# Kernel optimization log

Hardware: AMD Instinct MI355X
Metric: run time of the kernel (lower is better)

The kernel has to match this reference:

```python
import jax, jax.numpy as jnp
import numpy as np

NEG_SLOPE = 0.2
EPS = 1e-16  # matches PyG-style segment softmax denominator guard

N_NODES = 50000
N_EDGES = 800000
IN_CH = 256
HEADS = 4
OUT_CH = 32


def setup_inputs() -> dict:
    key = jax.random.key(0)
    k1, k2, k3, k4 = jax.random.split(key, 4)
    nodes_ft = jax.random.normal(k1, (N_NODES, IN_CH), dtype=jnp.float32)
    adj_list = jax.random.randint(k2, (2, N_EDGES), 0, N_NODES, dtype=jnp.int64)
    # xavier-normal-ish scales
    weight = jax.random.normal(k3, (IN_CH, HEADS * OUT_CH), dtype=jnp.float32) * (
        (2.0 / (IN_CH + HEADS * OUT_CH)) ** 0.5
    )
    att = jax.random.normal(k4, (1, HEADS, 2 * OUT_CH), dtype=jnp.float32) * (
        (2.0 / (1 + 2 * OUT_CH)) ** 0.5
    )
    bias = jnp.zeros((HEADS * OUT_CH,), dtype=jnp.float32)
    return {"nodes_ft": nodes_ft, "adj_list": adj_list, "weight": weight, "att": att, "bias": bias}


def reference(nodes_ft, adj_list, weight, att, bias):
    N = nodes_ft.shape[0]
    H, C = att.shape[1], att.shape[2] // 2
    dst = adj_list[0]  # softmax / aggregation key
    src = adj_list[1]
    # node hidden states: [N, H, C]
    h = (nodes_ft @ weight).reshape(N, H, C)
    xi = h[dst]  # [E, H, C]
    xj = h[src]  # [E, H, C]
    # attention logits: cat([xi, xj]) . att  ==  xi.att_i + xj.att_j
    att_i, att_j = att[:, :, :C], att[:, :, C:]
    alpha = (xi * att_i).sum(-1) + (xj * att_j).sum(-1)  # [E, H]
    alpha = jax.nn.leaky_relu(alpha, negative_slope=NEG_SLOPE)
    # segment softmax over destination node
    m = jax.ops.segment_max(alpha, dst, num_segments=N)  # [N, H]
    m = jnp.where(jnp.isfinite(m), m, 0.0)
    e = jnp.exp(alpha - m[dst])
    s = jax.ops.segment_sum(e, dst, num_segments=N)  # [N, H]
    a = e / (s[dst] + EPS)  # [E, H]
    # weighted scatter-add aggregate
    vals = xj * a[:, :, None]  # [E, H, C]
    out = jax.ops.segment_sum(vals, dst, num_segments=N)  # [N, H, C]
    out = out.reshape(N, H * C) + bias  # concat=True
    return out
```

## Files before the change

kernel.cpp:

```cpp
#include <hip/hip_runtime.h>
#include <hip/hip_bf16.h>
#include <math.h>

#define NN 50000
#define NE 800000
#define IN_CH 256
#define HEADS 4
#define OUT_CH 32
#define HC 128
#define NEG_SLOPE 0.2f
#define GAT_EPS 1e-16f

#define SBS 1024
#define NB  ((NN + SBS - 1) / SBS)

#define OFF_HB     0
#define OFF_WT     (NN*HC/2)
#define OFF_AI     (OFF_WT + 16384)
#define OFF_AJ     (OFF_AI + NN*HEADS)
#define OFF_ROW    (OFF_AJ + NN*HEADS)
#define OFF_CUR    (OFF_ROW + NN + 4)
#define OFF_HIST   (OFF_CUR + NN + 4)
#define OFF_BSUM   (OFF_HIST + NN + 4)
#define OFF_BOFF   (OFF_BSUM + NB + 4)
#define OFF_ESRC   (OFF_BOFF + NB + 4)

typedef __attribute__((ext_vector_type(8))) short short8v;
typedef __attribute__((ext_vector_type(4))) float float4v;

__device__ __forceinline__ unsigned short f2bf(float x) {
    union { float f; unsigned u; } v; v.f = x;
    unsigned r = v.u + 0x7fffu + ((v.u >> 16) & 1u);
    return (unsigned short)(r >> 16);
}
__device__ __forceinline__ float bf2f(unsigned short b) {
    union { unsigned u; float f; } v; v.u = ((unsigned)b) << 16;
    return v.f;
}

__global__ void k_zero(int* __restrict__ hist) {
    int i = blockIdx.x * blockDim.x + threadIdx.x;
    if (i < NN) hist[i] = 0;
}

__global__ void k_wt(const float* __restrict__ W, unsigned short* __restrict__ Wt) {
    int idx = blockIdx.x * blockDim.x + threadIdx.x;
    if (idx >= HC * IN_CH) return;
    int n = idx >> 8, k = idx & 255;
    Wt[n * IN_CH + k] = f2bf(W[(size_t)k * HC + n]);
}

__global__ __launch_bounds__(256) void k_gemm(const float* __restrict__ A,
                                              const unsigned short* __restrict__ Wt,
                                              unsigned short* __restrict__ Hb) {
    const int tid  = threadIdx.x;
    const int lane = tid & 63;
    const int w    = tid >> 6;
    const int wr   = w >> 1, wc = w & 1;
    const int blockRow = blockIdx.x * 128;

    const int lrow = lane & 15;
    const int kgrp = lane >> 4;

    float4v acc[4][4];
#pragma unroll
    for (int i = 0; i < 4; i++)
#pragma unroll
        for (int j = 0; j < 4; j++) acc[i][j] = (float4v){0.f, 0.f, 0.f, 0.f};

#pragma unroll
    for (int ks = 0; ks < 8; ks++) {
        const int kb = ks * 32 + kgrp * 8;
        short8v af[4], bfr[4];
#pragma unroll
        for (int mi = 0; mi < 4; mi++) {
            int r = blockRow + wr * 64 + mi * 16 + lrow;
            if (r >= NN) r = NN - 1;
            const float* ap = A + (size_t)r * IN_CH + kb;
            float4 a0 = *(const float4*)ap;
            float4 a1 = *(const float4*)(ap + 4);
            short8v t;
            t[0] = (short)f2bf(a0.x); t[1] = (short)f2bf(a0.y);
            t[2] = (short)f2bf(a0.z); t[3] = (short)f2bf(a0.w);
            t[4] = (short)f2bf(a1.x); t[5] = (short)f2bf(a1.y);
            t[6] = (short)f2bf(a1.z); t[7] = (short)f2bf(a1.w);
            af[mi] = t;
        }
#pragma unroll
        for (int ni = 0; ni < 4; ni++) {
            int c = wc * 64 + ni * 16 + lrow;
            bfr[ni] = *(const short8v*)(Wt + (size_t)c * IN_CH + kb);
        }
#pragma unroll
        for (int mi = 0; mi < 4; mi++)
#pragma unroll
            for (int ni = 0; ni < 4; ni++)
                acc[mi][ni] = __builtin_amdgcn_mfma_f32_16x16x32_bf16(
                    af[mi], bfr[ni], acc[mi][ni], 0, 0, 0);
    }

#pragma unroll
    for (int mi = 0; mi < 4; mi++) {
#pragma unroll
        for (int reg = 0; reg < 4; reg++) {
            int r = blockRow + wr * 64 + mi * 16 + kgrp * 4 + reg;
            if (r >= NN) continue;
#pragma unroll
            for (int ni = 0; ni < 4; ni++) {
                int c = wc * 64 + ni * 16 + lrow;
                Hb[(size_t)r * HC + c] = f2bf(acc[mi][ni][reg]);
            }
        }
    }
}

__global__ void k_att(const unsigned short* __restrict__ Hb, const float* __restrict__ att,
                      float* __restrict__ ai, float* __restrict__ aj) {
    int idx = blockIdx.x * blockDim.x + threadIdx.x;
    if (idx >= NN * HEADS) return;
    int n = idx >> 2, hh = idx & 3;
    const unsigned* hp = (const unsigned*)(Hb + (size_t)n * HC + hh * OUT_CH);
    const float* ati = att + hh * 2 * OUT_CH;
    const float* atj = ati + OUT_CH;
    float si = 0.f, sj = 0.f;
#pragma unroll
    for (int i = 0; i < 16; i++) {
        unsigned u = hp[i];
        float lo = bf2f((unsigned short)(u & 0xffff));
        float hi = bf2f((unsigned short)(u >> 16));
        si = fmaf(lo, ati[2 * i], si);     si = fmaf(hi, ati[2 * i + 1], si);
        sj = fmaf(lo, atj[2 * i], sj);     sj = fmaf(hi, atj[2 * i + 1], sj);
    }
    ai[idx] = si;
    aj[idx] = sj;
}

__global__ void k_hist(const int* __restrict__ adj, int* __restrict__ hist) {
    int e = blockIdx.x * blockDim.x + threadIdx.x;
    if (e < NE) atomicAdd(&hist[adj[e]], 1);
}

__global__ __launch_bounds__(256) void k_bsum(const int* __restrict__ hist,
                                              int* __restrict__ bsum) {
    int b = blockIdx.x, t = threadIdx.x;
    int i0 = b * SBS + t * 4;
    int s = 0;
#pragma unroll
    for (int j = 0; j < 4; j++) {
        int i = i0 + j;
        if (i < NN) s += hist[i];
    }
#pragma unroll
    for (int off = 32; off; off >>= 1) s += __shfl_xor(s, off);
    __shared__ int ws[4];
    int lane = t & 63, wid = t >> 6;
    if (lane == 0) ws[wid] = s;
    __syncthreads();
    if (t == 0) bsum[b] = ws[0] + ws[1] + ws[2] + ws[3];
}

__global__ __launch_bounds__(64) void k_bscan(const int* __restrict__ bsum,
                                              int* __restrict__ boff) {
    int lane = threadIdx.x;
    int v = (lane < NB) ? bsum[lane] : 0;
    int inc = v;
#pragma unroll
    for (int off = 1; off < 64; off <<= 1) {
        int u = __shfl_up(inc, off);
        if (lane >= off) inc += u;
    }
    if (lane < NB) boff[lane] = inc - v;
}

__global__ __launch_bounds__(256) void k_bwrite(const int* __restrict__ hist,
                                                const int* __restrict__ boff,
                                                int* __restrict__ row,
                                                int* __restrict__ cur) {
    int b = blockIdx.x, t = threadIdx.x;
    int i0 = b * SBS + t * 4;
    int v[4];
    int s = 0;
#pragma unroll
    for (int j = 0; j < 4; j++) {
        int i = i0 + j;
        v[j] = (i < NN) ? hist[i] : 0;
        s += v[j];
    }
    int lane = t & 63, wid = t >> 6;
    int inc = s;
#pragma unroll
    for (int off = 1; off < 64; off <<= 1) {
        int u = __shfl_up(inc, off);
        if (lane >= off) inc += u;
    }
    __shared__ int wsum[4];
    if (lane == 63) wsum[wid] = inc;
    __syncthreads();
    int woff = 0;
    for (int w2 = 0; w2 < wid; w2++) woff += wsum[w2];
    int run = boff[b] + woff + (inc - s);
#pragma unroll
    for (int j = 0; j < 4; j++) {
        int i = i0 + j;
        if (i < NN) {
            row[i] = run;
            cur[i] = run;
            run += v[j];
        }
    }
    if (b == 0 && t == 0) row[NN] = NE;
}

__global__ void k_scatter(const int* __restrict__ adj, int* __restrict__ cur,
                          int* __restrict__ esrc) {
    int e = blockIdx.x * blockDim.x + threadIdx.x;
    if (e >= NE) return;
    int dst = adj[e];
    int src = adj[NE + e];
    int pos = atomicAdd(&cur[dst], 1);
    esrc[pos] = src;
}

__device__ __forceinline__ float lrelu(float x) {
    return x > 0.f ? x : NEG_SLOPE * x;
}

__global__ __launch_bounds__(256) void k_gather(const int* __restrict__ row,
                                                const int* __restrict__ esrc,
                                                const float* __restrict__ ai,
                                                const float* __restrict__ aj,
                                                const unsigned short* __restrict__ Hb,
                                                const float* __restrict__ bias,
                                                float* __restrict__ out) {
    int gid = blockIdx.x * blockDim.x + threadIdx.x;
    int nid = gid >> 6;
    int lane = gid & 63;
    if (nid >= NN) return;
    int r0 = row[nid];
    int deg = row[nid + 1] - r0;

    float4 aiv = *(const float4*)&ai[nid * 4];

    float mx0 = -INFINITY, mx1 = -INFINITY, mx2 = -INFINITY, mx3 = -INFINITY;
    for (int k = lane; k < deg; k += 64) {
        int s = esrc[r0 + k];
        float4 ajv = *(const float4*)&aj[s * 4];
        mx0 = fmaxf(mx0, lrelu(aiv.x + ajv.x));
        mx1 = fmaxf(mx1, lrelu(aiv.y + ajv.y));
        mx2 = fmaxf(mx2, lrelu(aiv.z + ajv.z));
        mx3 = fmaxf(mx3, lrelu(aiv.w + ajv.w));
    }
#pragma unroll
    for (int off = 32; off; off >>= 1) {
        mx0 = fmaxf(mx0, __shfl_xor(mx0, off));
        mx1 = fmaxf(mx1, __shfl_xor(mx1, off));
        mx2 = fmaxf(mx2, __shfl_xor(mx2, off));
        mx3 = fmaxf(mx3, __shfl_xor(mx3, off));
    }

    float s0 = 0.f, s1 = 0.f, s2 = 0.f, s3 = 0.f;
    for (int k = lane; k < deg; k += 64) {
        int s = esrc[r0 + k];
        float4 ajv = *(const float4*)&aj[s * 4];
        s0 += __expf(lrelu(aiv.x + ajv.x) - mx0);
        s1 += __expf(lrelu(aiv.y + ajv.y) - mx1);
        s2 += __expf(lrelu(aiv.z + ajv.z) - mx2);
        s3 += __expf(lrelu(aiv.w + ajv.w) - mx3);
    }
#pragma unroll
    for (int off = 32; off; off >>= 1) {
        s0 += __shfl_xor(s0, off);
        s1 += __shfl_xor(s1, off);
        s2 += __shfl_xor(s2, off);
        s3 += __shfl_xor(s3, off);
    }

    int c0 = lane * 2;
    int hh = lane >> 4;
    float mh  = (hh & 2) ? ((hh & 1) ? mx3 : mx2) : ((hh & 1) ? mx1 : mx0);
    float sh  = (hh & 2) ? ((hh & 1) ? s3 : s2) : ((hh & 1) ? s1 : s0);
    float aih = (hh & 2) ? ((hh & 1) ? aiv.w : aiv.z) : ((hh & 1) ? aiv.y : aiv.x);
    float inv = 1.0f / (sh + GAT_EPS);

    float accx = 0.f, accy = 0.f;
#pragma unroll 4
    for (int k = 0; k < deg; k++) {
        int s = esrc[r0 + k];
        float al = lrelu(aih + aj[s * 4 + hh]);
        float a = __expf(al - mh) * inv;
        unsigned hu = *(const unsigned*)(Hb + (size_t)s * HC + c0);
        accx = fmaf(bf2f((unsigned short)(hu & 0xffff)), a, accx);
        accy = fmaf(bf2f((unsigned short)(hu >> 16)), a, accy);
    }
    out[(size_t)nid * HC + c0]     = accx + bias[c0];
    out[(size_t)nid * HC + c0 + 1] = accy + bias[c0 + 1];
}

extern "C" void kernel_launch(void* const* d_in, const int* in_sizes, int n_in,
                              void* d_out, int out_size, void* d_ws, size_t ws_size,
                              hipStream_t stream) {
    const float* nodes  = (const float*)d_in[0];
    const int*   adj    = (const int*)d_in[1];
    const float* weight = (const float*)d_in[2];
    const float* att    = (const float*)d_in[3];
    const float* bias   = (const float*)d_in[4];
    float* out = (float*)d_out;
    float* ws  = (float*)d_ws;

    unsigned short* Hb = (unsigned short*)(ws + OFF_HB);
    unsigned short* Wt = (unsigned short*)(ws + OFF_WT);
    float* ai   = ws + OFF_AI;
    float* aj   = ws + OFF_AJ;
    int*   rowp = (int*)(ws + OFF_ROW);
    int*   cur  = (int*)(ws + OFF_CUR);
    int*   hist = (int*)(ws + OFF_HIST);
    int*   bsum = (int*)(ws + OFF_BSUM);
    int*   boff = (int*)(ws + OFF_BOFF);
    int*   esrc = (int*)(ws + OFF_ESRC);

    k_zero<<<(NN + 255) / 256, 256, 0, stream>>>(hist);
    k_hist<<<(NE + 255) / 256, 256, 0, stream>>>(adj, hist);
    k_bsum<<<NB, 256, 0, stream>>>(hist, bsum);
    k_bscan<<<1, 64, 0, stream>>>(bsum, boff);
    k_bwrite<<<NB, 256, 0, stream>>>(hist, boff, rowp, cur);
    k_scatter<<<(NE + 255) / 256, 256, 0, stream>>>(adj, cur, esrc);
    k_wt<<<(HC * IN_CH + 255) / 256, 256, 0, stream>>>(weight, Wt);
    k_gemm<<<(NN + 127) / 128, 256, 0, stream>>>(nodes, Wt, Hb);
    k_att<<<(NN * HEADS + 255) / 256, 256, 0, stream>>>(Hb, att, ai, aj);
    k_gather<<<(NN * 64 + 255) / 256, 256, 0, stream>>>(rowp, esrc, ai, aj, Hb, bias, out);
}
```

Before: 296.7 us.

## Replace atomic CSR scatter with two-level binned counting sort

```diff
diff --git a/kernel.cpp b/kernel.cpp
--- a/kernel.cpp
+++ b/kernel.cpp
@@ -13,6 +13,12 @@
 
 #define SBS 1024
 #define NB  ((NN + SBS - 1) / SBS)
+
+#define NBINS 64
+#define BINSH 10
+#define NBBIN 49
+#define NBLK  625
+#define EPB   1280
 
 #define OFF_HB     0
 #define OFF_WT     (NN*HC/2)
@@ -23,7 +29,10 @@
 #define OFF_HIST   (OFF_CUR + NN + 4)
 #define OFF_BSUM   (OFF_HIST + NN + 4)
 #define OFF_BOFF   (OFF_BSUM + NB + 4)
-#define OFF_ESRC   (OFF_BOFF + NB + 4)
+#define OFF_BLKC   (OFF_BOFF + NB + 4)
+#define OFF_BLKO   (OFF_BLKC + NBLK*NBINS)
+#define OFF_PAIR   ((OFF_BLKO + NBLK*NBINS + 1) & ~1)
+#define OFF_ESRC   (OFF_PAIR + 2*NE)
 
 typedef __attribute__((ext_vector_type(8))) short short8v;
 typedef __attribute__((ext_vector_type(4))) float float4v;
@@ -135,9 +144,84 @@
     aj[idx] = sj;
 }
 
-__global__ void k_hist(const int* __restrict__ adj, int* __restrict__ hist) {
-    int e = blockIdx.x * blockDim.x + threadIdx.x;
-    if (e < NE) atomicAdd(&hist[adj[e]], 1);
+__global__ __launch_bounds__(256) void s_count(const int* __restrict__ adj,
+                                               int* __restrict__ hist,
+                                               int* __restrict__ blkcnt) {
+    __shared__ int lh[NBINS];
+    int b = blockIdx.x, t = threadIdx.x;
+    if (t < NBINS) lh[t] = 0;
+    __syncthreads();
+    int e0 = b * EPB;
+#pragma unroll
+    for (int i = 0; i < 5; i++) {
+        int e = e0 + i * 256 + t;
+        int dst = adj[e];
+        atomicAdd(&hist[dst], 1);
+        atomicAdd(&lh[dst >> BINSH], 1);
+    }
+    __syncthreads();
+    if (t < NBINS) blkcnt[b * NBINS + t] = lh[t];
+}
+
+__global__ __launch_bounds__(640) void s_scanblk(const int* __restrict__ blkcnt,
+                                                 int* __restrict__ blkoff) {
+    int bin = blockIdx.x, t = threadIdx.x;
+    int c = (t < NBLK) ? blkcnt[t * NBINS + bin] : 0;
+    int lane = t & 63, w = t >> 6;
+    int inc = c;
+#pragma unroll
+    for (int off = 1; off < 64; off <<= 1) {
+        int u = __shfl_up(inc, off);
+        if (lane >= off) inc += u;
+    }
+    __shared__ int wsum[10];
+    if (lane == 63) wsum[w] = inc;
+    __syncthreads();
+    int wpre = 0;
+    for (int i = 0; i < w; i++) wpre += wsum[i];
+    if (t < NBLK) blkoff[t * NBINS + bin] = wpre + inc - c;
+}
+
+__global__ __launch_bounds__(256) void s_pairs(const int* __restrict__ adj,
+                                               const int* __restrict__ rowp,
+                                               const int* __restrict__ blkoff,
+                                               int2* __restrict__ paired) {
+    __shared__ int lh[NBINS];
+    __shared__ int base[NBINS];
+    int b = blockIdx.x, t = threadIdx.x;
+    if (t < NBINS) {
+        lh[t] = 0;
+        int n0 = t << BINSH;
+        base[t] = rowp[n0 < NN ? n0 : NN] + blkoff[b * NBINS + t];
+    }
+    __syncthreads();
+    int e0 = b * EPB;
+#pragma unroll
+    for (int i = 0; i < 5; i++) {
+        int e = e0 + i * 256 + t;
+        int dst = adj[e];
+        int src = adj[NE + e];
+        int bin = dst >> BINSH;
+        int r = atomicAdd(&lh[bin], 1);
+        paired[base[bin] + r] = make_int2(dst, src);
+    }
+}
+
+__global__ __launch_bounds__(256) void s_csr(const int2* __restrict__ paired,
+                                             const int* __restrict__ rowp,
+                                             int* __restrict__ esrc) {
+    __shared__ int cur2[1 << BINSH];
+    int b = blockIdx.x, t = threadIdx.x;
+    for (int i = t; i < (1 << BINSH); i += 256) cur2[i] = 0;
+    __syncthreads();
+    int n0 = b << BINSH;
+    int n1 = n0 + (1 << BINSH); if (n1 > NN) n1 = NN;
+    int e0 = rowp[n0], e1 = rowp[n1];
+    for (int i = e0 + t; i < e1; i += 256) {
+        int2 p = paired[i];
+        int off = atomicAdd(&cur2[p.x - n0], 1);
+        esrc[rowp[p.x] + off] = p.y;
+    }
 }
 
 __global__ __launch_bounds__(256) void k_bsum(const int* __restrict__ hist,
@@ -209,16 +293,6 @@
         }
     }
     if (b == 0 && t == 0) row[NN] = NE;
-}
-
-__global__ void k_scatter(const int* __restrict__ adj, int* __restrict__ cur,
-                          int* __restrict__ esrc) {
-    int e = blockIdx.x * blockDim.x + threadIdx.x;
-    if (e >= NE) return;
-    int dst = adj[e];
-    int src = adj[NE + e];
-    int pos = atomicAdd(&cur[dst], 1);
-    esrc[pos] = src;
 }
 
 __device__ __forceinline__ float lrelu(float x) {
@@ -309,21 +383,26 @@
 
     unsigned short* Hb = (unsigned short*)(ws + OFF_HB);
     unsigned short* Wt = (unsigned short*)(ws + OFF_WT);
-    float* ai   = ws + OFF_AI;
-    float* aj   = ws + OFF_AJ;
-    int*   rowp = (int*)(ws + OFF_ROW);
-    int*   cur  = (int*)(ws + OFF_CUR);
-    int*   hist = (int*)(ws + OFF_HIST);
-    int*   bsum = (int*)(ws + OFF_BSUM);
-    int*   boff = (int*)(ws + OFF_BOFF);
-    int*   esrc = (int*)(ws + OFF_ESRC);
+    float* ai    = ws + OFF_AI;
+    float* aj    = ws + OFF_AJ;
+    int*   rowp  = (int*)(ws + OFF_ROW);
+    int*   cur   = (int*)(ws + OFF_CUR);
+    int*   hist  = (int*)(ws + OFF_HIST);
+    int*   bsum  = (int*)(ws + OFF_BSUM);
+    int*   boff  = (int*)(ws + OFF_BOFF);
+    int*   blkc  = (int*)(ws + OFF_BLKC);
+    int*   blko  = (int*)(ws + OFF_BLKO);
+    int2*  pair  = (int2*)(ws + OFF_PAIR);
+    int*   esrc  = (int*)(ws + OFF_ESRC);
 
     k_zero<<<(NN + 255) / 256, 256, 0, stream>>>(hist);
-    k_hist<<<(NE + 255) / 256, 256, 0, stream>>>(adj, hist);
+    s_count<<<NBLK, 256, 0, stream>>>(adj, hist, blkc);
     k_bsum<<<NB, 256, 0, stream>>>(hist, bsum);
     k_bscan<<<1, 64, 0, stream>>>(bsum, boff);
     k_bwrite<<<NB, 256, 0, stream>>>(hist, boff, rowp, cur);
-    k_scatter<<<(NE + 255) / 256, 256, 0, stream>>>(adj, cur, esrc);
+    s_scanblk<<<NBINS, 640, 0, stream>>>(blkc, blko);
+    s_pairs<<<NBLK, 256, 0, stream>>>(adj, rowp, blko, pair);
+    s_csr<<<NBBIN, 256, 0, stream>>>(pair, rowp, esrc);
     k_wt<<<(HC * IN_CH + 255) / 256, 256, 0, stream>>>(weight, Wt);
     k_gemm<<<(NN + 127) / 128, 256, 0, stream>>>(nodes, Wt, Hb);
     k_att<<<(NN * HEADS + 255) / 256, 256, 0, stream>>>(Hb, att, ai, aj);
```

After: 275.2 us. 7.2% less time.
